# Optimization experiments

Hardware: AMD Instinct MI355X
Metric: run time of the kernel (lower is better)

## Reference

```python
import jax, jax.numpy as jnp
import numpy as np

EPS = 1e-5

def setup_inputs() -> dict:
    key = jax.random.key(0)
    ks = jax.random.split(key, 10)
    B, N, K = 8, 16384, 16
    d = 4  # in_channels after concat (3 rel coords + 1 dist)
    coords = jax.random.normal(ks[0], (B, N, 3), dtype=jnp.float32)
    neighbor_coords = coords[:, :, None, :] + 0.1 * jax.random.normal(ks[1], (B, N, K, 3), dtype=jnp.float32)
    # SharedMLP(4, [4, 8]): Conv2d 1x1 (no bias, bn=True) + BN + ReLU, twice
    W1 = jax.random.normal(ks[2], (d, d), dtype=jnp.float32) * (1.0 / np.sqrt(d))
    g1 = jax.random.uniform(ks[3], (d,), dtype=jnp.float32, minval=0.5, maxval=1.5)
    b1 = jax.random.normal(ks[4], (d,), dtype=jnp.float32) * 0.1
    m1 = jax.random.normal(ks[5], (d,), dtype=jnp.float32) * 0.1
    v1 = jax.random.uniform(ks[5], (d,), dtype=jnp.float32, minval=0.5, maxval=1.5)
    W2 = jax.random.normal(ks[6], (2 * d, d), dtype=jnp.float32) * (1.0 / np.sqrt(d))
    g2 = jax.random.uniform(ks[7], (2 * d,), dtype=jnp.float32, minval=0.5, maxval=1.5)
    b2 = jax.random.normal(ks[8], (2 * d,), dtype=jnp.float32) * 0.1
    m2 = jax.random.normal(ks[9], (2 * d,), dtype=jnp.float32) * 0.1
    v2 = jax.random.uniform(ks[9], (2 * d,), dtype=jnp.float32, minval=0.5, maxval=1.5)
    return {"coords": coords, "neighbor_coords": neighbor_coords,
            "W1": W1, "g1": g1, "b1": b1, "m1": m1, "v1": v1,
            "W2": W2, "g2": g2, "b2": b2, "m2": m2, "v2": v2}

def _bn_relu(x, g, b, m, v):
    # inference batchnorm over channel (last) dim, fused with relu
    scale = g * jax.lax.rsqrt(v + EPS)
    return jax.nn.relu(x * scale + (b - m * scale))

def reference(coords, neighbor_coords, W1, g1, b1, m1, v1, W2, g2, b2, m2, v2):
    # relative coords + distance encoding: (B,N,K,4)
    rel = neighbor_coords - coords[:, :, None, :]
    dist = jnp.linalg.norm(rel, axis=-1, keepdims=True)
    enc = jnp.concatenate([rel, dist], axis=-1)
    # 1x1 conv == per-point matmul over channels (channels-last, no permute needed)
    h = _bn_relu(jnp.einsum('bnkc,oc->bnko', enc, W1), g1, b1, m1, v1)
    out = _bn_relu(jnp.einsum('bnkc,oc->bnko', h, W2), g2, b2, m2, v2)
    return out  # (B, N, K, 2*d)
```

## Files before the change

kernel.cpp:

```cpp
#include <hip/hip_runtime.h>

#define EPS 1e-5f

__global__ void fold_params(
    const float* __restrict__ W1, const float* __restrict__ g1,
    const float* __restrict__ b1, const float* __restrict__ m1,
    const float* __restrict__ v1,
    const float* __restrict__ W2, const float* __restrict__ g2,
    const float* __restrict__ b2, const float* __restrict__ m2,
    const float* __restrict__ v2,
    float* __restrict__ cst)
{
    if (threadIdx.x == 0 && blockIdx.x == 0) {
        for (int o = 0; o < 4; ++o) {
            float s = g1[o] * rsqrtf(v1[o] + EPS);
            for (int c = 0; c < 4; ++c) cst[o * 4 + c] = W1[o * 4 + c] * s;
            cst[16 + o] = b1[o] - m1[o] * s;
        }
        for (int o = 0; o < 8; ++o) {
            float s = g2[o] * rsqrtf(v2[o] + EPS);
            for (int c = 0; c < 4; ++c) cst[20 + o * 4 + c] = W2[o * 4 + c] * s;
            cst[52 + o] = b2[o] - m2[o] * s;
        }
    }
}

__global__ __launch_bounds__(256) void lse_kernel(
    const float* __restrict__ coords,
    const float* __restrict__ nbr,
    const float* __restrict__ cst,
    float* __restrict__ out,
    int total)
{
    int tid = blockIdx.x * blockDim.x + threadIdx.x;
    if (tid >= total) return;

    int bn = tid >> 4;
    float cx = coords[bn * 3 + 0];
    float cy = coords[bn * 3 + 1];
    float cz = coords[bn * 3 + 2];
    float rx = nbr[(size_t)tid * 3 + 0] - cx;
    float ry = nbr[(size_t)tid * 3 + 1] - cy;
    float rz = nbr[(size_t)tid * 3 + 2] - cz;
    float dist = sqrtf(rx * rx + ry * ry + rz * rz);
    float enc[4] = {rx, ry, rz, dist};

    float h[4];
#pragma unroll
    for (int o = 0; o < 4; ++o) {
        float a = cst[16 + o];
#pragma unroll
        for (int c = 0; c < 4; ++c) a = fmaf(cst[o * 4 + c], enc[c], a);
        h[o] = fmaxf(a, 0.f);
    }

    float r[8];
#pragma unroll
    for (int o = 0; o < 8; ++o) {
        float a = cst[52 + o];
#pragma unroll
        for (int c = 0; c < 4; ++c) a = fmaf(cst[20 + o * 4 + c], h[c], a);
        r[o] = fmaxf(a, 0.f);
    }

    float4* op = (float4*)(out + (size_t)tid * 8);
    op[0] = make_float4(r[0], r[1], r[2], r[3]);
    op[1] = make_float4(r[4], r[5], r[6], r[7]);
}

extern "C" void kernel_launch(void* const* d_in, const int* in_sizes, int n_in,
                              void* d_out, int out_size, void* d_ws, size_t ws_size,
                              hipStream_t stream) {
    const float* coords = (const float*)d_in[0];
    const float* nbr    = (const float*)d_in[1];
    float* cst = (float*)d_ws;
    float* out = (float*)d_out;

    fold_params<<<1, 64, 0, stream>>>((const float*)d_in[2], (const float*)d_in[3],
                                      (const float*)d_in[4], (const float*)d_in[5],
                                      (const float*)d_in[6], (const float*)d_in[7],
                                      (const float*)d_in[8], (const float*)d_in[9],
                                      (const float*)d_in[10], (const float*)d_in[11],
                                      cst);

    int total = in_sizes[1] / 3;
    int block = 256;
    int grid = (total + block - 1) / block;
    lse_kernel<<<grid, block, 0, stream>>>(coords, nbr, cst, out, total);
}
```

Before: 117.0 us.

## Fuse BN parameter folding into main kernel and process four neighbors per thread

Removes the separate single-thread fold_params launch. Each thread now recomputes the folded weights and biases in registers from the raw BN parameters. Each thread also handles four neighbors, loading their coordinates as three float4 vectors and writing eight float4 outputs. The aim is to cut the extra launch and its serial dependency and to widen the loads. The cost is redundant per-thread parameter work, more registers, and output stores that are strided across lanes.

Result: slower. 123.6 us (+5.6%).

```diff
diff --git a/kernel.cpp b/kernel.cpp
--- a/kernel.cpp
+++ b/kernel.cpp
@@ -2,70 +2,79 @@
 
 #define EPS 1e-5f
 
-__global__ void fold_params(
+__global__ __launch_bounds__(256) void lse_kernel(
+    const float*  __restrict__ coords,
+    const float4* __restrict__ nbr4,
     const float* __restrict__ W1, const float* __restrict__ g1,
     const float* __restrict__ b1, const float* __restrict__ m1,
     const float* __restrict__ v1,
     const float* __restrict__ W2, const float* __restrict__ g2,
     const float* __restrict__ b2, const float* __restrict__ m2,
     const float* __restrict__ v2,
-    float* __restrict__ cst)
+    float4* __restrict__ out4,
+    int quads)
 {
-    if (threadIdx.x == 0 && blockIdx.x == 0) {
-        for (int o = 0; o < 4; ++o) {
-            float s = g1[o] * rsqrtf(v1[o] + EPS);
-            for (int c = 0; c < 4; ++c) cst[o * 4 + c] = W1[o * 4 + c] * s;
-            cst[16 + o] = b1[o] - m1[o] * s;
-        }
-        for (int o = 0; o < 8; ++o) {
-            float s = g2[o] * rsqrtf(v2[o] + EPS);
-            for (int c = 0; c < 4; ++c) cst[20 + o * 4 + c] = W2[o * 4 + c] * s;
-            cst[52 + o] = b2[o] - m2[o] * s;
-        }
+    int q = blockIdx.x * blockDim.x + threadIdx.x;
+    if (q >= quads) return;
+
+    float w1f[16], sh1[4];
+#pragma unroll
+    for (int o = 0; o < 4; ++o) {
+        float s = g1[o] * rsqrtf(v1[o] + EPS);
+#pragma unroll
+        for (int c = 0; c < 4; ++c) w1f[o * 4 + c] = W1[o * 4 + c] * s;
+        sh1[o] = b1[o] - m1[o] * s;
     }
-}
+    float w2f[32], sh2[8];
+#pragma unroll
+    for (int o = 0; o < 8; ++o) {
+        float s = g2[o] * rsqrtf(v2[o] + EPS);
+#pragma unroll
+        for (int c = 0; c < 4; ++c) w2f[o * 4 + c] = W2[o * 4 + c] * s;
+        sh2[o] = b2[o] - m2[o] * s;
+    }
 
-__global__ __launch_bounds__(256) void lse_kernel(
-    const float* __restrict__ coords,
-    const float* __restrict__ nbr,
-    const float* __restrict__ cst,
-    float* __restrict__ out,
-    int total)
-{
-    int tid = blockIdx.x * blockDim.x + threadIdx.x;
-    if (tid >= total) return;
-
-    int bn = tid >> 4;
+    int bn = q >> 2;
     float cx = coords[bn * 3 + 0];
     float cy = coords[bn * 3 + 1];
     float cz = coords[bn * 3 + 2];
-    float rx = nbr[(size_t)tid * 3 + 0] - cx;
-    float ry = nbr[(size_t)tid * 3 + 1] - cy;
-    float rz = nbr[(size_t)tid * 3 + 2] - cz;
-    float dist = sqrtf(rx * rx + ry * ry + rz * rz);
-    float enc[4] = {rx, ry, rz, dist};
 
-    float h[4];
+    float4 p0 = nbr4[(size_t)q * 3 + 0];
+    float4 p1 = nbr4[(size_t)q * 3 + 1];
+    float4 p2 = nbr4[(size_t)q * 3 + 2];
+    float nb[12] = {p0.x, p0.y, p0.z, p0.w,
+                    p1.x, p1.y, p1.z, p1.w,
+                    p2.x, p2.y, p2.z, p2.w};
+
 #pragma unroll
-    for (int o = 0; o < 4; ++o) {
-        float a = cst[16 + o];
+    for (int k = 0; k < 4; ++k) {
+        float rx = nb[k * 3 + 0] - cx;
+        float ry = nb[k * 3 + 1] - cy;
+        float rz = nb[k * 3 + 2] - cz;
+        float dist = sqrtf(rx * rx + ry * ry + rz * rz);
+        float enc[4] = {rx, ry, rz, dist};
+
+        float h[4];
 #pragma unroll
-        for (int c = 0; c < 4; ++c) a = fmaf(cst[o * 4 + c], enc[c], a);
-        h[o] = fmaxf(a, 0.f);
+        for (int o = 0; o < 4; ++o) {
+            float a = sh1[o];
+#pragma unroll
+            for (int c = 0; c < 4; ++c) a = fmaf(w1f[o * 4 + c], enc[c], a);
+            h[o] = fmaxf(a, 0.f);
+        }
+
+        float r[8];
+#pragma unroll
+        for (int o = 0; o < 8; ++o) {
+            float a = sh2[o];
+#pragma unroll
+            for (int c = 0; c < 4; ++c) a = fmaf(w2f[o * 4 + c], h[c], a);
+            r[o] = fmaxf(a, 0.f);
+        }
+
+        out4[(size_t)q * 8 + k * 2 + 0] = make_float4(r[0], r[1], r[2], r[3]);
+        out4[(size_t)q * 8 + k * 2 + 1] = make_float4(r[4], r[5], r[6], r[7]);
     }
-
-    float r[8];
-#pragma unroll
-    for (int o = 0; o < 8; ++o) {
-        float a = cst[52 + o];
-#pragma unroll
-        for (int c = 0; c < 4; ++c) a = fmaf(cst[20 + o * 4 + c], h[c], a);
-        r[o] = fmaxf(a, 0.f);
-    }
-
-    float4* op = (float4*)(out + (size_t)tid * 8);
-    op[0] = make_float4(r[0], r[1], r[2], r[3]);
-    op[1] = make_float4(r[4], r[5], r[6], r[7]);
 }
 
 extern "C" void kernel_launch(void* const* d_in, const int* in_sizes, int n_in,
@@ -73,18 +82,17 @@
                               hipStream_t stream) {
     const float* coords = (const float*)d_in[0];
     const float* nbr    = (const float*)d_in[1];
-    float* cst = (float*)d_ws;
     float* out = (float*)d_out;
 
-    fold_params<<<1, 64, 0, stream>>>((const float*)d_in[2], (const float*)d_in[3],
-                                      (const float*)d_in[4], (const float*)d_in[5],
-                                      (const float*)d_in[6], (const float*)d_in[7],
-                                      (const float*)d_in[8], (const float*)d_in[9],
-                                      (const float*)d_in[10], (const float*)d_in[11],
-                                      cst);
-
     int total = in_sizes[1] / 3;
+    int quads = total >> 2;
     int block = 256;
-    int grid = (total + block - 1) / block;
-    lse_kernel<<<grid, block, 0, stream>>>(coords, nbr, cst, out, total);
+    int grid = (quads + block - 1) / block;
+    lse_kernel<<<grid, block, 0, stream>>>(
+        coords, (const float4*)nbr,
+        (const float*)d_in[2], (const float*)d_in[3], (const float*)d_in[4],
+        (const float*)d_in[5], (const float*)d_in[6],
+        (const float*)d_in[7], (const float*)d_in[8], (const float*)d_in[9],
+        (const float*)d_in[10], (const float*)d_in[11],
+        (float4*)out, quads);
 }
```

## Fold BN params inside main kernel and use grid-stride loop

Applied to the files above, without the earlier changes.

Removes the separate single-thread fold_params launch and instead has every thread fold weights and batchnorm parameters into registers, made wave-uniform with readfirstlane. The main kernel becomes a grid-stride loop over a fixed 2048-block grid, so the per-thread folding cost is amortized over several elements. This drops one kernel launch and its serial dependency. In exchange every thread redundantly loads and folds the parameters, and register use rises because 60 folded constants are held per thread.

Measured after the change: 118.5 us. Within noise of the previous version (+1.3%).

```diff
diff --git a/kernel.cpp b/kernel.cpp
--- a/kernel.cpp
+++ b/kernel.cpp
@@ -2,70 +2,72 @@
 
 #define EPS 1e-5f
 
-__global__ void fold_params(
+__device__ __forceinline__ float rfl(float x) {
+    return __int_as_float(__builtin_amdgcn_readfirstlane(__float_as_int(x)));
+}
+
+__global__ __launch_bounds__(256) void lse_kernel(
+    const float* __restrict__ coords,
+    const float* __restrict__ nbr,
     const float* __restrict__ W1, const float* __restrict__ g1,
     const float* __restrict__ b1, const float* __restrict__ m1,
     const float* __restrict__ v1,
     const float* __restrict__ W2, const float* __restrict__ g2,
     const float* __restrict__ b2, const float* __restrict__ m2,
     const float* __restrict__ v2,
-    float* __restrict__ cst)
-{
-    if (threadIdx.x == 0 && blockIdx.x == 0) {
-        for (int o = 0; o < 4; ++o) {
-            float s = g1[o] * rsqrtf(v1[o] + EPS);
-            for (int c = 0; c < 4; ++c) cst[o * 4 + c] = W1[o * 4 + c] * s;
-            cst[16 + o] = b1[o] - m1[o] * s;
-        }
-        for (int o = 0; o < 8; ++o) {
-            float s = g2[o] * rsqrtf(v2[o] + EPS);
-            for (int c = 0; c < 4; ++c) cst[20 + o * 4 + c] = W2[o * 4 + c] * s;
-            cst[52 + o] = b2[o] - m2[o] * s;
-        }
-    }
-}
-
-__global__ __launch_bounds__(256) void lse_kernel(
-    const float* __restrict__ coords,
-    const float* __restrict__ nbr,
-    const float* __restrict__ cst,
     float* __restrict__ out,
     int total)
 {
-    int tid = blockIdx.x * blockDim.x + threadIdx.x;
-    if (tid >= total) return;
-
-    int bn = tid >> 4;
-    float cx = coords[bn * 3 + 0];
-    float cy = coords[bn * 3 + 1];
-    float cz = coords[bn * 3 + 2];
-    float rx = nbr[(size_t)tid * 3 + 0] - cx;
-    float ry = nbr[(size_t)tid * 3 + 1] - cy;
-    float rz = nbr[(size_t)tid * 3 + 2] - cz;
-    float dist = sqrtf(rx * rx + ry * ry + rz * rz);
-    float enc[4] = {rx, ry, rz, dist};
-
-    float h[4];
+    float w1f[16], sh1[4], w2f[32], sh2[8];
 #pragma unroll
     for (int o = 0; o < 4; ++o) {
-        float a = cst[16 + o];
+        float s = g1[o] * rsqrtf(v1[o] + EPS);
 #pragma unroll
-        for (int c = 0; c < 4; ++c) a = fmaf(cst[o * 4 + c], enc[c], a);
-        h[o] = fmaxf(a, 0.f);
+        for (int c = 0; c < 4; ++c) w1f[o * 4 + c] = rfl(W1[o * 4 + c] * s);
+        sh1[o] = rfl(b1[o] - m1[o] * s);
+    }
+#pragma unroll
+    for (int o = 0; o < 8; ++o) {
+        float s = g2[o] * rsqrtf(v2[o] + EPS);
+#pragma unroll
+        for (int c = 0; c < 4; ++c) w2f[o * 4 + c] = rfl(W2[o * 4 + c] * s);
+        sh2[o] = rfl(b2[o] - m2[o] * s);
     }
 
-    float r[8];
+    const int stride = gridDim.x * blockDim.x;
+    for (int tid = blockIdx.x * blockDim.x + threadIdx.x; tid < total; tid += stride) {
+        int bn = tid >> 4;
+        float cx = coords[bn * 3 + 0];
+        float cy = coords[bn * 3 + 1];
+        float cz = coords[bn * 3 + 2];
+        float rx = nbr[(size_t)tid * 3 + 0] - cx;
+        float ry = nbr[(size_t)tid * 3 + 1] - cy;
+        float rz = nbr[(size_t)tid * 3 + 2] - cz;
+        float dist = sqrtf(rx * rx + ry * ry + rz * rz);
+        float enc[4] = {rx, ry, rz, dist};
+
+        float h[4];
 #pragma unroll
-    for (int o = 0; o < 8; ++o) {
-        float a = cst[52 + o];
+        for (int o = 0; o < 4; ++o) {
+            float a = sh1[o];
 #pragma unroll
-        for (int c = 0; c < 4; ++c) a = fmaf(cst[20 + o * 4 + c], h[c], a);
-        r[o] = fmaxf(a, 0.f);
+            for (int c = 0; c < 4; ++c) a = fmaf(w1f[o * 4 + c], enc[c], a);
+            h[o] = fmaxf(a, 0.f);
+        }
+
+        float r[8];
+#pragma unroll
+        for (int o = 0; o < 8; ++o) {
+            float a = sh2[o];
+#pragma unroll
+            for (int c = 0; c < 4; ++c) a = fmaf(w2f[o * 4 + c], h[c], a);
+            r[o] = fmaxf(a, 0.f);
+        }
+
+        float4* op = (float4*)(out + (size_t)tid * 8);
+        op[0] = make_float4(r[0], r[1], r[2], r[3]);
+        op[1] = make_float4(r[4], r[5], r[6], r[7]);
     }
-
-    float4* op = (float4*)(out + (size_t)tid * 8);
-    op[0] = make_float4(r[0], r[1], r[2], r[3]);
-    op[1] = make_float4(r[4], r[5], r[6], r[7]);
 }
 
 extern "C" void kernel_launch(void* const* d_in, const int* in_sizes, int n_in,
@@ -73,18 +75,16 @@
                               hipStream_t stream) {
     const float* coords = (const float*)d_in[0];
     const float* nbr    = (const float*)d_in[1];
-    float* cst = (float*)d_ws;
     float* out = (float*)d_out;
-
-    fold_params<<<1, 64, 0, stream>>>((const float*)d_in[2], (const float*)d_in[3],
-                                      (const float*)d_in[4], (const float*)d_in[5],
-                                      (const float*)d_in[6], (const float*)d_in[7],
-                                      (const float*)d_in[8], (const float*)d_in[9],
-                                      (const float*)d_in[10], (const float*)d_in[11],
-                                      cst);
 
     int total = in_sizes[1] / 3;
     int block = 256;
-    int grid = (total + block - 1) / block;
-    lse_kernel<<<grid, block, 0, stream>>>(coords, nbr, cst, out, total);
+    int grid  = 2048;
+    lse_kernel<<<grid, block, 0, stream>>>(
+        coords, nbr,
+        (const float*)d_in[2], (const float*)d_in[3], (const float*)d_in[4],
+        (const float*)d_in[5], (const float*)d_in[6],
+        (const float*)d_in[7], (const float*)d_in[8], (const float*)d_in[9],
+        (const float*)d_in[10], (const float*)d_in[11],
+        out, total);
 }
```
